# Optimization experiments

Hardware: AMD Instinct MI355X
Metric: run time of the kernel (lower is better)

Reference implementation:

```python
import jax, jax.numpy as jnp
import numpy as np

jax.config.update("jax_enable_x64", True)  # loss accumulates int64 squared index diffs (~1e14)

PATCH, STRIDE = 7, 1


def extract_patches(img, p, s):
    # img: [b, c, h, w] -> patches [b, N, c*p*p], N = oh*ow (normalize_patch='none')
    pat = jax.lax.conv_general_dilated_patches(img, (p, p), (s, s), 'VALID')  # [b, c*p*p, oh, ow]
    b, d = pat.shape[0], pat.shape[1]
    return pat.reshape(b, d, -1).transpose(0, 2, 1)


def bisect_left(a, v):
    # Exact replica of np.searchsorted(a, v, side='left') binary search,
    # applied (as in the original code) to an UNSORTED int array `a`.
    # a: [N] int, v: [M] int -> [M] insertion indices in [0, N].
    N = a.shape[0]
    lo = jnp.zeros(v.shape, jnp.int64)
    hi = jnp.full(v.shape, N, jnp.int64)
    n_iter = int(np.ceil(np.log2(N))) + 1
    for _ in range(n_iter):
        mid = (lo + hi) // 2
        am = a[jnp.clip(mid, 0, N - 1)]
        go = lo < hi
        pred = am < v
        lo = jnp.where(go & pred, mid + 1, lo)
        hi = jnp.where(go & (~pred), mid, hi)
    return lo


def nearest_vals(a, v):
    # Vectorized find_nearest(a, v_i) for all v_i. a: [N], v: [M].
    N = a.shape[0]
    idx = bisect_left(a, v)
    a_prev = a[jnp.clip(idx - 1, 0, N - 1)]
    a_at = a[jnp.clip(idx, 0, N - 1)]
    take_prev = (idx > 0) & ((idx == N) | (jnp.abs(v - a_prev) < jnp.abs(v - a_at)))
    return jnp.where(take_prev, a_prev, a_at)


def reference(x, y, rand):
    # rand: [b, d, num_proj]; per-batch projection matrix, normalized by unbiased column std
    rand = rand / jnp.std(rand, axis=1, keepdims=True, ddof=1)
    xp = extract_patches(x, PATCH, STRIDE)  # [b, N, d]
    yp = extract_patches(y, PATCH, STRIDE)  # [b, N, d]
    proj_x = jnp.einsum('bnd,bdp->bnp', xp, rand)
    proj_y = jnp.einsum('bnd,bdp->bnp', yp, rand)
    # Original overwrites projections with argsort indices; only j=0 is used
    # because of the early return inside the projection loop.
    ai = jnp.argsort(proj_x[:, :, 0], axis=1).astype(jnp.int64)  # [b, N]
    at = jnp.argsort(proj_y[:, :, 0], axis=1).astype(jnp.int64)  # [b, N]
    nearest = jax.vmap(nearest_vals)(at, ai)  # [b, N]
    N = ai.shape[1]
    per_image = jnp.sum((ai - nearest) ** 2, axis=1) / N  # int sum -> float
    return jnp.mean(per_image)  # batch_reduction='mean'


def setup_inputs() -> dict:
    key = jax.random.key(0)
    k1, k2, k3 = jax.random.split(key, 3)
    b, c, h, w = 4, 3, 256, 256
    d = c * PATCH * PATCH  # 147
    x = jax.random.normal(k1, (b, c, h, w), dtype=jnp.float32)
    y = jax.random.normal(k2, (b, c, h, w), dtype=jnp.float32)
    rand = jax.random.normal(k3, (b, d, 1), dtype=jnp.float32)
    return {"x": x, "y": y, "rand": rand}
```

## Files before the change

kernel.cpp:

```cpp
#include <hip/hip_runtime.h>
#include <stdint.h>

#define OH 250
#define OW 250
#define NPTS (OH*OW)
#define NSEG 4
#define D 147
#define CH 3
#define IMH 256
#define IMW 256
#define NITER 17
#define NBUCK 8192
#define CAP 128
#define SIG0 12.124355652982141

typedef unsigned long long u64;
typedef unsigned int u32;

#define OFF_SREC  0UL
#define OFF_A     33554432UL
#define OFF_CURS  34559136UL
#define OFF_SUMS  34821296UL
#define OFF_TICK  34821328UL
#define OFF_OFLOW 34821336UL
#define WS_NEED   34821340UL
#define ZERO_BYTES (WS_NEED - OFF_CURS)

__device__ __forceinline__ u64 packd(double f) {
  u64 u = (u64)__double_as_longlong(f);
  return (u & 0x8000000000000000ULL) ? ~u : (u | 0x8000000000000000ULL);
}

__device__ __forceinline__ int bucket_of(u64 rec) {
  u64 t = rec & ~0x1FFFFULL;
  u64 bits = (t & 0x8000000000000000ULL) ? (t & 0x7FFFFFFFFFFFFFFFULL) : ~t;
  double v = __longlong_as_double((long long)bits);
  double z = (v + 4.0 * SIG0) * ((double)NBUCK / (8.0 * SIG0));
  int b = (z <= 0.0) ? 0 : (int)z;
  if (b > NBUCK - 1) b = NBUCK - 1;
  return b;
}

__global__ __launch_bounds__(256) void conv_kern(const float* __restrict__ y,
                                                 const float* __restrict__ rnd,
                                                 u64* __restrict__ srec,
                                                 u32* __restrict__ curs,
                                                 u32* __restrict__ oflow) {
  __shared__ float tile[CH][22][22];
  __shared__ double wlds[D];
  int b = blockIdx.z;
  int tid = threadIdx.y * 16 + threadIdx.x;
  int lane = tid & 63;
  {
    const float* rb = rnd + b * D;
    double v0 = (double)rb[lane];
    double v1 = (double)rb[lane + 64];
    double v2 = (lane + 128 < D) ? (double)rb[lane + 128] : 0.0;
    double sm = v0 + v1 + v2;
    #pragma unroll
    for (int o = 32; o > 0; o >>= 1) sm += __shfl_xor(sm, o, 64);
    double mean = sm / (double)D;
    double d0 = v0 - mean, d1 = v1 - mean;
    double d2 = (lane + 128 < D) ? (v2 - mean) : 0.0;
    double ss = d0 * d0 + d1 * d1 + d2 * d2;
    #pragma unroll
    for (int o = 32; o > 0; o >>= 1) ss += __shfl_xor(ss, o, 64);
    double stdv = sqrt(ss / (double)(D - 1));
    if (tid < 64) {
      wlds[lane] = v0 / stdv;
      wlds[lane + 64] = v1 / stdv;
      if (lane + 128 < D) wlds[lane + 128] = v2 / stdv;
    }
  }
  const float* in = y + (size_t)b * CH * IMH * IMW;
  int bi = blockIdx.y * 16, bj = blockIdx.x * 16;
  for (int c = 0; c < CH; ++c)
    for (int t = tid; t < 22 * 22; t += 256) {
      int rr = t / 22, cc = t - rr * 22;
      int r = bi + rr, col = bj + cc;
      float v = 0.f;
      if (r < IMH && col < IMW) v = in[((size_t)c * IMH + r) * IMW + col];
      tile[c][rr][cc] = v;
    }
  __syncthreads();
  int i = bi + threadIdx.y, j = bj + threadIdx.x;
  if (i < OH && j < OW) {
    double acc = 0.0;
    #pragma unroll
    for (int c = 0; c < CH; ++c) {
      double ac = 0.0;
      #pragma unroll
      for (int ph = 0; ph < 7; ++ph)
        #pragma unroll
        for (int pw = 0; pw < 7; ++pw)
          ac = fma((double)tile[c][threadIdx.y + ph][threadIdx.x + pw],
                   wlds[c * 49 + ph * 7 + pw], ac);
      acc += ac;
    }
    int n = i * OW + j;
    u64 rec = (packd(acc) & ~0x1FFFFULL) | (u64)(u32)n;
    int bk = b * NBUCK + bucket_of(rec);
    u32 pos = atomicAdd(&curs[bk], 1u);
    if (pos < CAP) srec[(size_t)bk * CAP + pos] = rec;
    else atomicOr(oflow, 1u);
  }
}

__global__ __launch_bounds__(512) void bsort_kern(const u64* __restrict__ srec,
                                                  const u32* __restrict__ curs,
                                                  u32* __restrict__ a,
                                                  u32* __restrict__ oflow) {
  __shared__ u32 bases_s[NBUCK];
  __shared__ u64 buf[8][CAP];
  __shared__ u32 wsum[8];
  int tid = threadIdx.x;
  int wid = tid >> 6, lane = tid & 63;
  int seg = blockIdx.x >> 10;
  const u32* cs = curs + seg * NBUCK;
  u32 c[16]; u32 run = 0;
  #pragma unroll
  for (int m = 0; m < 16; ++m) {
    u32 v = cs[tid * 16 + m];
    c[m] = v > CAP ? CAP : v;
    run += c[m];
  }
  u32 inc = run;
  #pragma unroll
  for (int o = 1; o < 64; o <<= 1) {
    u32 v = __shfl_up(inc, o, 64);
    if (lane >= o) inc += v;
  }
  if (lane == 63) wsum[wid] = inc;
  __syncthreads();
  u32 woff = 0;
  for (int w2 = 0; w2 < wid; ++w2) woff += wsum[w2];
  u32 ex = woff + inc - run;
  #pragma unroll
  for (int m = 0; m < 16; ++m) {
    bases_s[tid * 16 + m] = ex;
    ex += c[m];
  }
  if (tid == 511 && ex != NPTS) atomicOr(oflow, 2u);
  __syncthreads();
  int B = blockIdx.x * 8 + wid;
  int bk = B & (NBUCK - 1);
  u32 v = cs[bk];
  int n = (int)(v > CAP ? CAP : v);
  const u64* src = srec + (size_t)B * CAP;
  u32* dst = a + (size_t)seg * NPTS + bases_s[bk];
  for (int i = lane; i < n; i += 64) buf[wid][i] = src[i];
  __syncthreads();
  for (int i = lane; i < n; i += 64) {
    u64 x = buf[wid][i];
    int r = 0;
    for (int j = 0; j < n; ++j) r += (buf[wid][j] < x);
    dst[r] = (u32)(x & 0x1FFFFULL);
  }
}

#define HALF (NSEG * NPTS / 2)
__global__ __launch_bounds__(256) void loss_kern(const u32* __restrict__ a_all,
                                                 u64* __restrict__ sums,
                                                 u32* __restrict__ tick,
                                                 const u32* __restrict__ oflow,
                                                 float* __restrict__ out,
                                                 int nblocks) {
  __shared__ u64 lsums[NSEG];
  __shared__ u32 rank_s;
  int tid = threadIdx.x;
  if (tid < NSEG) lsums[tid] = 0ULL;
  __syncthreads();
  int g = blockIdx.x * 256 + tid;
  if (g < HALF) {
    int g1 = g + HALF;
    int s0 = g / NPTS, s1 = g1 / NPTS;
    int vv0 = g - s0 * NPTS, vv1 = g1 - s1 * NPTS;
    const u32* A0 = a_all + (size_t)s0 * NPTS;
    const u32* A1 = a_all + (size_t)s1 * NPTS;
    int lo0 = 0, hi0 = NPTS, lo1 = 0, hi1 = NPTS;
    #pragma unroll
    for (int it = 0; it < NITER; ++it) {
      int mid0 = (lo0 + hi0) >> 1, mid1 = (lo1 + hi1) >> 1;
      int cm0 = mid0 > NPTS - 1 ? NPTS - 1 : mid0;
      int cm1 = mid1 > NPTS - 1 ? NPTS - 1 : mid1;
      int am0 = (int)A0[cm0];
      int am1 = (int)A1[cm1];
      if (lo0 < hi0) { if (am0 < vv0) lo0 = mid0 + 1; else hi0 = mid0; }
      if (lo1 < hi1) { if (am1 < vv1) lo1 = mid1 + 1; else hi1 = mid1; }
    }
    {
      int pi = lo0 - 1; if (pi < 0) pi = 0; if (pi > NPTS - 1) pi = NPTS - 1;
      int ci = lo0;     if (ci > NPTS - 1) ci = NPTS - 1;
      int ap = (int)A0[pi], aa = (int)A0[ci];
      int d1 = vv0 - ap; if (d1 < 0) d1 = -d1;
      int d2 = vv0 - aa; if (d2 < 0) d2 = -d2;
      bool tp = (lo0 > 0) && ((lo0 == NPTS) || (d1 < d2));
      long long dd = (long long)(vv0 - (tp ? ap : aa));
      atomicAdd(&lsums[s0], (u64)(dd * dd));
    }
    {
      int pi = lo1 - 1; if (pi < 0) pi = 0; if (pi > NPTS - 1) pi = NPTS - 1;
      int ci = lo1;     if (ci > NPTS - 1) ci = NPTS - 1;
      int ap = (int)A1[pi], aa = (int)A1[ci];
      int d1 = vv1 - ap; if (d1 < 0) d1 = -d1;
      int d2 = vv1 - aa; if (d2 < 0) d2 = -d2;
      bool tp = (lo1 > 0) && ((lo1 == NPTS) || (d1 < d2));
      long long dd = (long long)(vv1 - (tp ? ap : aa));
      atomicAdd(&lsums[s1], (u64)(dd * dd));
    }
  }
  __syncthreads();
  if (tid < NSEG && lsums[tid]) atomicAdd(&sums[tid], lsums[tid]);
  __syncthreads();
  if (tid == 0) {
    rank_s = atomicAdd(&tick[1], 1u);
    if (rank_s == (u32)(nblocks - 1)) {
      u32 of = __hip_atomic_load(oflow, __ATOMIC_RELAXED, __HIP_MEMORY_SCOPE_AGENT);
      if (of) { out[0] = 8.0e12f + 1.0e11f * (float)of; return; }
      double l = 0.0;
      for (int s = 0; s < NSEG; ++s) {
        u64 sv = __hip_atomic_load(&sums[s], __ATOMIC_RELAXED, __HIP_MEMORY_SCOPE_AGENT);
        l += (double)(long long)sv / (double)NPTS;
      }
      out[0] = (float)(l / 4.0);
    }
  }
}

__global__ void guard_kern(float* __restrict__ out) {
  if (threadIdx.x == 0 && blockIdx.x == 0) out[0] = 9.0e12f;
}

extern "C" void kernel_launch(void* const* d_in, const int* in_sizes, int n_in,
                              void* d_out, int out_size, void* d_ws, size_t ws_size,
                              hipStream_t stream) {
  (void)in_sizes; (void)n_in; (void)out_size;
  if (ws_size < WS_NEED) { guard_kern<<<1, 64, 0, stream>>>((float*)d_out); return; }
  const float* y   = (const float*)d_in[1];
  const float* rnd = (const float*)d_in[2];

  char* ws = (char*)d_ws;
  u64* srec   = (u64*)(ws + OFF_SREC);
  u32* aidx   = (u32*)(ws + OFF_A);
  u32* curs   = (u32*)(ws + OFF_CURS);
  u64* sums   = (u64*)(ws + OFF_SUMS);
  u32* tick   = (u32*)(ws + OFF_TICK);
  u32* oflow  = (u32*)(ws + OFF_OFLOW);
  float* out  = (float*)d_out;

  hipMemsetAsync(ws + OFF_CURS, 0, ZERO_BYTES, stream);
  conv_kern<<<dim3(16, 16, NSEG), dim3(16, 16), 0, stream>>>(y, rnd, srec, curs, oflow);
  bsort_kern<<<NSEG * NBUCK / 8, 512, 0, stream>>>(srec, curs, aidx, oflow);
  int nb = (HALF + 255) / 256;
  loss_kern<<<nb, 256, 0, stream>>>(aidx, sums, tick, oflow, out, nb);
}
```

Before: 129.3 us.

## Replace memset with setup kernel, precompute weights, batch buckets per wave in bsort

A small setup kernel now zeroes the counters and computes the normalized projection weights once per batch, replacing the hipMemsetAsync and the per-block std computation in the conv kernel. The bucket sort kernel drops from 4096 blocks to 512, with each wave handling 8 buckets and prefetching their records into registers. This cuts the redundant prefix-scan work that every block repeated and the per-bucket block-wide syncs. The cost is fewer blocks and more registers per thread, which may reduce occupancy.

```diff
diff --git a/kernel.cpp b/kernel.cpp
--- a/kernel.cpp
+++ b/kernel.cpp
@@ -19,12 +19,12 @@
 
 #define OFF_SREC  0UL
 #define OFF_A     33554432UL
+#define OFF_WTS   34554432UL
 #define OFF_CURS  34559136UL
 #define OFF_SUMS  34821296UL
 #define OFF_TICK  34821328UL
 #define OFF_OFLOW 34821336UL
 #define WS_NEED   34821340UL
-#define ZERO_BYTES (WS_NEED - OFF_CURS)
 
 __device__ __forceinline__ u64 packd(double f) {
   u64 u = (u64)__double_as_longlong(f);
@@ -41,39 +41,57 @@
   return b;
 }
 
+__global__ __launch_bounds__(256) void setup_kern(const float* __restrict__ rnd,
+                                                  double* __restrict__ wts,
+                                                  u32* __restrict__ curs,
+                                                  u64* __restrict__ sums,
+                                                  u32* __restrict__ tick,
+                                                  u32* __restrict__ oflow) {
+  int t = threadIdx.x;
+  if (blockIdx.x < 4) {
+    int b = blockIdx.x;
+    int lane = t & 63;
+    double v0 = (double)rnd[b * D + lane];
+    double v1 = (double)rnd[b * D + lane + 64];
+    double v2 = (lane + 128 < D) ? (double)rnd[b * D + lane + 128] : 0.0;
+    double sm = v0 + v1 + v2;
+    #pragma unroll
+    for (int o = 32; o > 0; o >>= 1) sm += __shfl_xor(sm, o, 64);
+    double mean = sm / (double)D;
+    double d0 = v0 - mean, d1 = v1 - mean;
+    double d2 = (lane + 128 < D) ? (v2 - mean) : 0.0;
+    double ss = d0 * d0 + d1 * d1 + d2 * d2;
+    #pragma unroll
+    for (int o = 32; o > 0; o >>= 1) ss += __shfl_xor(ss, o, 64);
+    double stdv = sqrt(ss / (double)(D - 1));
+    if (t < 64) {
+      wts[b * D + lane] = v0 / stdv;
+      wts[b * D + lane + 64] = v1 / stdv;
+      if (lane + 128 < D) wts[b * D + lane + 128] = v2 / stdv;
+    }
+    if (b == 0 && t < 8) ((u32*)sums)[t] = 0u;
+    if (b == 0 && t >= 8 && t < 10) tick[t - 8] = 0u;
+    if (b == 0 && t == 10) oflow[0] = 0u;
+  } else {
+    int g = (blockIdx.x - 4) * 1024 + t * 4;
+    if (g < NSEG * NBUCK) {
+      curs[g] = 0u; curs[g + 1] = 0u; curs[g + 2] = 0u; curs[g + 3] = 0u;
+    }
+  }
+}
+
 __global__ __launch_bounds__(256) void conv_kern(const float* __restrict__ y,
-                                                 const float* __restrict__ rnd,
+                                                 const double* __restrict__ wts,
                                                  u64* __restrict__ srec,
                                                  u32* __restrict__ curs,
                                                  u32* __restrict__ oflow) {
   __shared__ float tile[CH][22][22];
   __shared__ double wlds[D];
   int b = blockIdx.z;
-  int tid = threadIdx.y * 16 + threadIdx.x;
-  int lane = tid & 63;
-  {
-    const float* rb = rnd + b * D;
-    double v0 = (double)rb[lane];
-    double v1 = (double)rb[lane + 64];
-    double v2 = (lane + 128 < D) ? (double)rb[lane + 128] : 0.0;
-    double sm = v0 + v1 + v2;
-    #pragma unroll
-    for (int o = 32; o > 0; o >>= 1) sm += __shfl_xor(sm, o, 64);
-    double mean = sm / (double)D;
-    double d0 = v0 - mean, d1 = v1 - mean;
-    double d2 = (lane + 128 < D) ? (v2 - mean) : 0.0;
-    double ss = d0 * d0 + d1 * d1 + d2 * d2;
-    #pragma unroll
-    for (int o = 32; o > 0; o >>= 1) ss += __shfl_xor(ss, o, 64);
-    double stdv = sqrt(ss / (double)(D - 1));
-    if (tid < 64) {
-      wlds[lane] = v0 / stdv;
-      wlds[lane + 64] = v1 / stdv;
-      if (lane + 128 < D) wlds[lane + 128] = v2 / stdv;
-    }
-  }
   const float* in = y + (size_t)b * CH * IMH * IMW;
   int bi = blockIdx.y * 16, bj = blockIdx.x * 16;
+  int tid = threadIdx.y * 16 + threadIdx.x;
+  if (tid < D) wlds[tid] = wts[b * D + tid];
   for (int c = 0; c < CH; ++c)
     for (int t = tid; t < 22 * 22; t += 256) {
       int rr = t / 22, cc = t - rr * 22;
@@ -115,46 +133,63 @@
   __shared__ u32 wsum[8];
   int tid = threadIdx.x;
   int wid = tid >> 6, lane = tid & 63;
-  int seg = blockIdx.x >> 10;
+  int seg = blockIdx.x >> 7;
   const u32* cs = curs + seg * NBUCK;
-  u32 c[16]; u32 run = 0;
+  {
+    u32 c[16]; u32 run = 0;
+    #pragma unroll
+    for (int m = 0; m < 16; ++m) {
+      u32 v = cs[tid * 16 + m];
+      c[m] = v > CAP ? CAP : v;
+      run += c[m];
+    }
+    u32 inc = run;
+    #pragma unroll
+    for (int o = 1; o < 64; o <<= 1) {
+      u32 v = __shfl_up(inc, o, 64);
+      if (lane >= o) inc += v;
+    }
+    if (lane == 63) wsum[wid] = inc;
+    __syncthreads();
+    u32 woff = 0;
+    for (int w2 = 0; w2 < wid; ++w2) woff += wsum[w2];
+    u32 ex = woff + inc - run;
+    #pragma unroll
+    for (int m = 0; m < 16; ++m) {
+      bases_s[tid * 16 + m] = ex;
+      ex += c[m];
+    }
+    if (tid == 511 && ex != NPTS) atomicOr(oflow, 2u);
+  }
+  __syncthreads();
+  int bk0 = (blockIdx.x & 127) * 64 + wid * 8;
+  u64 x0[8], x1[8]; int nn[8];
   #pragma unroll
-  for (int m = 0; m < 16; ++m) {
-    u32 v = cs[tid * 16 + m];
-    c[m] = v > CAP ? CAP : v;
-    run += c[m];
-  }
-  u32 inc = run;
+  for (int k = 0; k < 8; ++k) {
+    int bk = bk0 + k;
+    u32 v = cs[bk];
+    int n = (int)(v > CAP ? CAP : v);
+    nn[k] = n;
+    const u64* src = srec + (size_t)(seg * NBUCK + bk) * CAP;
+    x0[k] = (lane < n) ? src[lane] : ~0ULL;
+    x1[k] = (lane + 64 < n) ? src[lane + 64] : ~0ULL;
+  }
+  u32* aseg = a + (size_t)seg * NPTS;
   #pragma unroll
-  for (int o = 1; o < 64; o <<= 1) {
-    u32 v = __shfl_up(inc, o, 64);
-    if (lane >= o) inc += v;
-  }
-  if (lane == 63) wsum[wid] = inc;
-  __syncthreads();
-  u32 woff = 0;
-  for (int w2 = 0; w2 < wid; ++w2) woff += wsum[w2];
-  u32 ex = woff + inc - run;
-  #pragma unroll
-  for (int m = 0; m < 16; ++m) {
-    bases_s[tid * 16 + m] = ex;
-    ex += c[m];
-  }
-  if (tid == 511 && ex != NPTS) atomicOr(oflow, 2u);
-  __syncthreads();
-  int B = blockIdx.x * 8 + wid;
-  int bk = B & (NBUCK - 1);
-  u32 v = cs[bk];
-  int n = (int)(v > CAP ? CAP : v);
-  const u64* src = srec + (size_t)B * CAP;
-  u32* dst = a + (size_t)seg * NPTS + bases_s[bk];
-  for (int i = lane; i < n; i += 64) buf[wid][i] = src[i];
-  __syncthreads();
-  for (int i = lane; i < n; i += 64) {
-    u64 x = buf[wid][i];
-    int r = 0;
-    for (int j = 0; j < n; ++j) r += (buf[wid][j] < x);
-    dst[r] = (u32)(x & 0x1FFFFULL);
+  for (int k = 0; k < 8; ++k) {
+    int n = nn[k];
+    if (n <= 0) continue;
+    if (lane < n) buf[wid][lane] = x0[k];
+    if (lane + 64 < n) buf[wid][lane + 64] = x1[k];
+    int r0 = 0, r1 = 0;
+    for (int j = 0; j < n; ++j) {
+      u64 bj = buf[wid][j];
+      r0 += (bj < x0[k]);
+      r1 += (bj < x1[k]);
+    }
+    u32* dst = aseg + bases_s[bk0 + k];
+    if (lane < n) dst[r0] = (u32)(x0[k] & 0x1FFFFULL);
+    if (lane + 64 < n) dst[r1] = (u32)(x1[k] & 0x1FFFFULL);
   }
 }
 
@@ -242,15 +277,16 @@
   char* ws = (char*)d_ws;
   u64* srec   = (u64*)(ws + OFF_SREC);
   u32* aidx   = (u32*)(ws + OFF_A);
+  double* wts = (double*)(ws + OFF_WTS);
   u32* curs   = (u32*)(ws + OFF_CURS);
   u64* sums   = (u64*)(ws + OFF_SUMS);
   u32* tick   = (u32*)(ws + OFF_TICK);
   u32* oflow  = (u32*)(ws + OFF_OFLOW);
   float* out  = (float*)d_out;
 
-  hipMemsetAsync(ws + OFF_CURS, 0, ZERO_BYTES, stream);
-  conv_kern<<<dim3(16, 16, NSEG), dim3(16, 16), 0, stream>>>(y, rnd, srec, curs, oflow);
-  bsort_kern<<<NSEG * NBUCK / 8, 512, 0, stream>>>(srec, curs, aidx, oflow);
+  setup_kern<<<36, 256, 0, stream>>>(rnd, wts, curs, sums, tick, oflow);
+  conv_kern<<<dim3(16, 16, NSEG), dim3(16, 16), 0, stream>>>(y, wts, srec, curs, oflow);
+  bsort_kern<<<512, 512, 0, stream>>>(srec, curs, aidx, oflow);
   int nb = (HALF + 255) / 256;
   loss_kern<<<nb, 256, 0, stream>>>(aidx, sums, tick, oflow, out, nb);
 }
```

Measured after the change: 123.8 us. -4.3%, faster.
